# Optimization experiments

Hardware: AMD Instinct MI355X
Metric: run time of the kernel (lower is better)

The kernel has to match this reference:

```python
import jax, jax.numpy as jnp
import numpy as np

B, L, N = 8, 720, 321
D_MODEL, H, E_LAYERS, PRED = 512, 8, 2, 336
D_HEAD = D_MODEL // H
D_FF = 128
FACTOR = 5
U = min(int(FACTOR * np.ceil(np.log(L))), L)  # = 35: top-u queries and sample size
EPS = 1e-5


def _layer_norm(x, g, b):
    mu = x.mean(-1, keepdims=True)
    var = ((x - mu) ** 2).mean(-1, keepdims=True)
    return (x - mu) / jnp.sqrt(var + EPS) * g + b


def _prob_attention(q, k, v, samp_idx):
    # Informer ProbSparse attention (mask_flag=False). q,k,v: [B,H,L,Dh]
    Bq, Hq, Lq, Dh = q.shape
    k_samp = k[:, :, samp_idx, :]                                   # [B,H,L,S,Dh]
    qk_samp = jnp.einsum('bhld,bhlsd->bhls', q, k_samp)             # sampled scores
    M = qk_samp.max(-1) - qk_samp.sum(-1) / Lq                      # sparsity measure
    _, m_top = jax.lax.top_k(M, U)                                  # [B,H,U]
    q_red = jnp.take_along_axis(q, m_top[..., None], axis=2)        # [B,H,U,Dh]
    scores = jnp.einsum('bhud,bhld->bhul', q_red, k) * (1.0 / np.sqrt(Dh))
    attn = jax.nn.softmax(scores, axis=-1)
    upd = jnp.einsum('bhul,bhld->bhud', attn, v)                    # [B,H,U,Dh]
    ctx = jnp.broadcast_to(v.mean(axis=2, keepdims=True), q.shape)  # mean-V init
    b_idx = jnp.arange(Bq)[:, None, None]
    h_idx = jnp.arange(Hq)[None, :, None]
    return ctx.at[b_idx, h_idx, m_top].set(upd)


def _forward(x_enc, embed_w, embed_b, wq, bq, wk, bk, wv, bv, wo, bo,
             ln1_g, ln1_b, w1, b1, w2, b2, ln2_g, ln2_b,
             wout, bout, wg, bg, samp_idx):
    x = jnp.transpose(x_enc, (0, 2, 1))                             # [B,N,L]
    mean = x.mean(-1, keepdims=True)
    std = jnp.std(x, axis=-1, ddof=1, keepdims=True) + EPS
    xs = (x - mean) / std
    h = jnp.transpose(xs, (0, 2, 1)) @ embed_w + embed_b            # [B,L,Dm]
    y = jnp.zeros((B, L, PRED), dtype=h.dtype)

    def heads(t):
        return jnp.transpose(t.reshape(B, L, H, D_HEAD), (0, 2, 1, 3))

    for l in range(E_LAYERS):
        q = heads(h @ wq[l] + bq[l])
        k = heads(h @ wk[l] + bk[l])
        v = heads(h @ wv[l] + bv[l])
        ctx = _prob_attention(q, k, v, samp_idx)
        ctx = jnp.transpose(ctx, (0, 2, 1, 3)).reshape(B, L, D_MODEL)
        attn_out = ctx @ wo[l] + bo[l]
        hx = _layer_norm(h - attn_out, ln1_g[l], ln1_b[l])          # Minusformer subtraction
        ff = jax.nn.relu(hx @ w1[l] + b1[l]) @ w2[l] + b2[l]
        h = _layer_norm(hx - ff, ln2_g[l], ln2_b[l])
        y = y + (h @ wout[l] + bout[l]) * jax.nn.sigmoid(h @ wg[l] + bg[l])
    out = y[:, :N, :] * std + mean                                  # inverse scaling [B,N,PRED]
    return jnp.transpose(out, (0, 2, 1))                            # [B,PRED,N]


def setup_inputs() -> dict:
    key = jax.random.key(0)
    ks = jax.random.split(key, 12)
    s = 0.02

    def w(k, shape):
        return jax.random.normal(k, shape, dtype=jnp.float32) * s

    return {
        'x_enc': jax.random.normal(ks[0], (B, L, N), dtype=jnp.float32),
        'samp_idx': jax.random.randint(ks[1], (L, U), 0, L),
        'embed_w': w(ks[2], (N, D_MODEL)),
        'embed_b': jnp.zeros((D_MODEL,), jnp.float32),
        'wq': w(ks[3], (E_LAYERS, D_MODEL, D_MODEL)),
        'bq': jnp.zeros((E_LAYERS, D_MODEL), jnp.float32),
        'wk': w(ks[4], (E_LAYERS, D_MODEL, D_MODEL)),
        'bk': jnp.zeros((E_LAYERS, D_MODEL), jnp.float32),
        'wv': w(ks[5], (E_LAYERS, D_MODEL, D_MODEL)),
        'bv': jnp.zeros((E_LAYERS, D_MODEL), jnp.float32),
        'wo': w(ks[6], (E_LAYERS, D_MODEL, D_MODEL)),
        'bo': jnp.zeros((E_LAYERS, D_MODEL), jnp.float32),
        'ln1_g': jnp.ones((E_LAYERS, D_MODEL), jnp.float32),
        'ln1_b': jnp.zeros((E_LAYERS, D_MODEL), jnp.float32),
        'w1': w(ks[7], (E_LAYERS, D_MODEL, D_FF)),
        'b1': jnp.zeros((E_LAYERS, D_FF), jnp.float32),
        'w2': w(ks[8], (E_LAYERS, D_FF, D_MODEL)),
        'b2': jnp.zeros((E_LAYERS, D_MODEL), jnp.float32),
        'ln2_g': jnp.ones((E_LAYERS, D_MODEL), jnp.float32),
        'ln2_b': jnp.zeros((E_LAYERS, D_MODEL), jnp.float32),
        'wout': w(ks[9], (E_LAYERS, D_MODEL, PRED)),
        'bout': jnp.zeros((E_LAYERS, PRED), jnp.float32),
        'wg': w(ks[10], (E_LAYERS, D_MODEL, PRED)),
        'bg': jnp.zeros((E_LAYERS, PRED), jnp.float32),
    }


def reference(x_enc, samp_idx, embed_w, embed_b, wq, bq, wk, bk, wv, bv, wo, bo,
              ln1_g, ln1_b, w1, b1, w2, b2, ln2_g, ln2_b, wout, bout, wg, bg):
    return _forward(x_enc, embed_w, embed_b, wq, bq, wk, bk, wv, bv, wo, bo,
                    ln1_g, ln1_b, w1, b1, w2, b2, ln2_g, ln2_b,
                    wout, bout, wg, bg, samp_idx)
```

## Files before the change

kernel.cpp:

```cpp
#include <hip/hip_runtime.h>
#include <math.h>

#define BB_ 8
#define LL_ 720
#define NF 321
#define DM 512
#define HH_ 8
#define DH 64
#define DFF 128
#define PRED 336
#define UK 35
#define NLAY 2
#define EPSF 1e-5f
#define BL (BB_*LL_)
#define TJC 72
#define NCH (LL_/TJC)
#define LCH 48
#define NLC (LL_/LCH)

typedef unsigned short ushort;
typedef __attribute__((ext_vector_type(4))) float f32x4;
typedef __attribute__((ext_vector_type(8))) ushort ushort8;
typedef __attribute__((ext_vector_type(4))) ushort ushortx4;

#define KVSEG ((size_t)64*LL_*64)

__device__ __forceinline__ float b2f(ushort u){
  unsigned int x = ((unsigned int)u) << 16;
  return __builtin_bit_cast(float, x);
}
__device__ __forceinline__ ushort f2b(float f){
  unsigned int x = __builtin_bit_cast(unsigned int, f);
  unsigned int r = x + 0x7fff + ((x >> 16) & 1);
  return (ushort)(r >> 16);
}

__device__ __forceinline__ float wredsum(float v){
#pragma unroll
  for (int o=32;o>0;o>>=1) v += __shfl_xor(v,o,64);
  return v;
}
__device__ __forceinline__ float wredmax(float v){
#pragma unroll
  for (int o=32;o>0;o>>=1) v = fmaxf(v,__shfl_xor(v,o,64));
  return v;
}
__device__ __forceinline__ float bredsum(float v, float* red){
  int lane = threadIdx.x & 63, wid = threadIdx.x >> 6;
  v = wredsum(v);
  __syncthreads();
  if (lane==0) red[wid]=v;
  __syncthreads();
  return red[0]+red[1]+red[2]+red[3];
}

__global__ __launch_bounds__(256) void stats3_k(const float* __restrict__ x,
                                                float* __restrict__ pp){
  __shared__ float s1[4][64], s2[4][64];
  int blk = blockIdx.x;
  int lc = blk % NLC; int r = blk / NLC;
  int nt = r % 6; int b = r / 6;
  int nl = threadIdx.x & 63, lg = threadIdx.x >> 6;
  int n = nt*64 + nl;
  float sum=0.f, ss=0.f;
  if (n < NF){
    const float* xp = x + ((size_t)b*LL_ + lc*LCH)*NF + n;
    for (int l=lg; l<LCH; l+=4){ float v = xp[(size_t)l*NF]; sum += v; ss = fmaf(v,v,ss); }
  }
  s1[lg][nl]=sum; s2[lg][nl]=ss;
  __syncthreads();
  if (lg==0){
    float S = s1[0][nl]+s1[1][nl]+s1[2][nl]+s1[3][nl];
    float Q = s2[0][nl]+s2[1][nl]+s2[2][nl]+s2[3][nl];
    pp[(size_t)blk*128 + nl]      = S;
    pp[(size_t)blk*128 + 64 + nl] = Q;
  }
}

__global__ __launch_bounds__(64) void statsc_k(const float* __restrict__ pp,
                                               float* __restrict__ mean,
                                               float* __restrict__ stdv,
                                               float* __restrict__ rstd){
  int bn6 = blockIdx.x;
  int nl = threadIdx.x;
  int nt = bn6 % 6, b = bn6 / 6;
  int n = nt*64 + nl;
  if (n >= NF) return;
  float S=0.f, Q=0.f;
#pragma unroll
  for (int lc=0; lc<NLC; ++lc){
    size_t base = ((size_t)(b*6+nt)*NLC + lc)*128;
    S += pp[base + nl];
    Q += pp[base + 64 + nl];
  }
  float mu = S*(1.f/LL_);
  float var = fmaxf((Q - S*mu)*(1.f/(LL_-1)), 0.f);
  float sd = sqrtf(var) + EPSF;
  int bn = b*NF+n;
  mean[bn]=mu; stdv[bn]=sd; rstd[bn]=1.f/sd;
}

#define KPE 352
__global__ __launch_bounds__(256) void xnorm_k(const float* __restrict__ x,
                                               const float* __restrict__ mean,
                                               const float* __restrict__ rstd,
                                               ushort* __restrict__ xn){
  int idx = blockIdx.x*256 + threadIdx.x;
  if (idx >= BL*KPE) return;
  int c = idx % KPE; int bl = idx / KPE; int b = bl / LL_;
  float v = 0.f;
  if (c < NF) v = (x[(size_t)bl*NF + c] - mean[b*NF+c]) * rstd[b*NF+c];
  xn[idx] = f2b(v);
}

struct TDesc { const float* in; ushort* out; int N, K, Npad, Kpad, nbx, blk0, ilv; };
struct TPack { TDesc d[17]; int n; };
__global__ __launch_bounds__(256) void transpose_k(TPack p){
  __shared__ float tile[32][33];
  int blk = blockIdx.x;
  int di = 0;
  while (di+1 < p.n && p.d[di+1].blk0 <= blk) ++di;
  TDesc D = p.d[di];
  int rel = blk - D.blk0;
  int bx = rel % D.nbx, by = rel / D.nbx;
  int k0 = bx*32, n0 = by*32;
  int t = threadIdx.x; int tx = t & 31, ty = t >> 5;
#pragma unroll
  for (int i=0;i<4;++i){
    int k = k0+ty+8*i, n = n0+tx;
    float v = (k < D.K && n < D.N) ? D.in[(size_t)k*D.N + n] : 0.f;
    tile[ty+8*i][tx] = v;
  }
  __syncthreads();
#pragma unroll
  for (int i=0;i<4;++i){
    int n = n0+ty+8*i, k = k0+tx;
    if (n < D.Npad && k < D.Kpad){
      int outn = D.ilv ? (2*n + (D.ilv-1)) : n;
      D.out[(size_t)outn*D.Kpad + k] = f2b(tile[tx][ty+8*i]);
    }
  }
}

__global__ __launch_bounds__(256) void pack_bias_k(const float* __restrict__ bq,
                                                   const float* __restrict__ bk,
                                                   const float* __restrict__ bv,
                                                   const float* __restrict__ bo2,
                                                   const float* __restrict__ bg,
                                                   float* __restrict__ bqkv,
                                                   float* __restrict__ bog){
  int t = blockIdx.x*256 + threadIdx.x;
  if (t < 2*1536){
    int l = t/1536, c = t%1536;
    float v = c<512 ? bq[l*512+c] : (c<1024 ? bk[l*512+c-512] : bv[l*512+c-1024]);
    bqkv[t] = v;
  }
  if (t < 2*672){
    int l = t/672, c = t%672;
    int p = c>>1;
    bog[t] = (c&1) ? bg[l*336+p] : bo2[l*336+p];
  }
}

__global__ __launch_bounds__(256) void gemm_k(
    const ushort* __restrict__ A, const ushort* __restrict__ Bt,
    const float* __restrict__ bias, void* __restrict__ Cout,
    ushort* __restrict__ Cbf, ushort* __restrict__ kvp,
    int N, int K, int flags)
{
  __shared__ ushort As[128*32];
  __shared__ ushort Bs[128*32];
  const int t = threadIdx.x;
  const int bm = blockIdx.y << 7, bn = blockIdx.x << 7;
  const int lane = t & 63, wid = t >> 6;
  const int wm = (wid >> 1) << 6, wn = (wid & 1) << 6;
  const int fr = lane & 15, kg = lane >> 4;

  f32x4 acc[4][4];
#pragma unroll
  for (int i=0;i<4;++i)
#pragma unroll
    for (int j=0;j<4;++j) acc[i][j] = (f32x4){0.f,0.f,0.f,0.f};

  const int rA0 = t >> 2,        qA0 = t & 3;
  const int rA1 = (t+256) >> 2;
  const size_t aOff0 = (size_t)(bm + rA0)*K + qA0*8;
  const size_t aOff1 = (size_t)(bm + rA1)*K + qA0*8;
  const size_t bOff0 = (size_t)(bn + rA0)*K + qA0*8;
  const size_t bOff1 = (size_t)(bn + rA1)*K + qA0*8;
  const int lA0 = (rA0<<5) + ((qA0 ^ ((rA0>>1)&3))<<3);
  const int lA1 = (rA1<<5) + ((qA0 ^ ((rA1>>1)&3))<<3);

  for (int k0=0; k0<K; k0+=32){
    ushort8 va0 = *(const ushort8*)(A  + aOff0 + k0);
    ushort8 va1 = *(const ushort8*)(A  + aOff1 + k0);
    ushort8 vb0 = *(const ushort8*)(Bt + bOff0 + k0);
    ushort8 vb1 = *(const ushort8*)(Bt + bOff1 + k0);
    *(ushort8*)&As[lA0] = va0;
    *(ushort8*)&As[lA1] = va1;
    *(ushort8*)&Bs[lA0] = vb0;
    *(ushort8*)&Bs[lA1] = vb1;
    __syncthreads();
    ushort8 af[4], bfr[4];
#pragma unroll
    for (int i=0;i<4;++i){
      int ra = wm + (i<<4) + fr;
      af[i]  = *(const ushort8*)&As[(ra<<5) + ((kg ^ ((ra>>1)&3))<<3)];
      int rb = wn + (i<<4) + fr;
      bfr[i] = *(const ushort8*)&Bs[(rb<<5) + ((kg ^ ((rb>>1)&3))<<3)];
    }
#pragma unroll
    for (int i=0;i<4;++i)
#pragma unroll
      for (int j=0;j<4;++j)
        asm("v_mfma_f32_16x16x32_bf16 %0, %1, %2, %0"
            : "+v"(acc[i][j]) : "v"(af[i]), "v"(bfr[j]));
    __syncthreads();
  }

  const int colBase = bn + wn + fr;
  const int rowBase = bm + wm + (kg << 2);

  if (flags & 16){
#pragma unroll
    for (int j=0;j<4;++j){
      int col = colBase + (j<<4);
      if (col >= N) continue;
      float bv = bias[col];
#pragma unroll
      for (int i=0;i<4;++i){
        int row0 = rowBase + (i<<4);
#pragma unroll
        for (int r=0;r<4;++r){
          float v = acc[i][j][r] + bv;
          float o = __shfl_xor(v, 1, 64);
          if ((lane & 1) == 0){
            float val = v * (1.f/(1.f+__expf(-o)));
            size_t yi = (size_t)(row0+r)*PRED + (col>>1);
            float* yp = (float*)Cout;
            yp[yi] = (flags & 32) ? (yp[yi] + val) : val;
          }
        }
      }
    }
    return;
  }

#pragma unroll
  for (int j=0;j<4;++j){
    int col = colBase + (j<<4);
    if (col >= N) continue;
    float bv = bias[col];
#pragma unroll
    for (int i=0;i<4;++i){
      int row0 = rowBase + (i<<4);
#pragma unroll
      for (int r=0;r<4;++r){
        float v = acc[i][j][r] + bv;
        if (flags & 1) v = fmaxf(v, 0.f);
        int row = row0 + r;
        size_t idx = (size_t)row*N + col;
        if (flags & 2) ((ushort*)Cout)[idx] = f2b(v);
        else if (flags & 8){
          if (col < 512) ((float*)Cout)[idx] = v;
          else {
            int hh = (col >> 6) & 7;
            int dd = col & 63;
            int bb = row / LL_; int jr = row - bb*LL_;
            ushort bfv = f2b(v);
            if (col < 1024)
              kvp[((size_t)(bb*8+hh)*LL_ + jr)*64 + dd] = bfv;
            else
              kvp[KVSEG + ((size_t)(bb*8+hh)*LL_ + jr)*64 + dd] = bfv;
          }
        } else {
          ((float*)Cout)[idx] = v;
          if (flags & 4) Cbf[idx] = f2b(v);
        }
      }
    }
  }
}

__global__ __launch_bounds__(256) void msc_k(const float* __restrict__ qkv,
                                             const ushort* __restrict__ kR,
                                             const int* __restrict__ samp,
                                             float* __restrict__ Mb){
  __shared__ float sq[4][64];
  int wid = threadIdx.x >> 6, lane = threadIdx.x & 63;
  int gid = blockIdx.x*4 + wid;
  int l = gid % LL_; int bh = gid / LL_; int h = bh & 7; int b = bh >> 3;
  sq[wid][lane] = qkv[(size_t)(b*LL_ + l)*1536 + h*64 + lane];
  __syncthreads();
  float acc = 0.f;
  if (lane < UK){
    int j = samp[l*UK + lane];
    const ushort8* kr = (const ushort8*)(kR + ((size_t)bh*LL_ + j)*64);
    const float* sqw = sq[wid];
#pragma unroll
    for (int d8=0; d8<8; ++d8){
      ushort8 kk = kr[d8];
#pragma unroll
      for (int e=0;e<8;++e) acc = fmaf(sqw[d8*8+e], b2f(kk[e]), acc);
    }
  }
  float mx = (lane < UK) ? acc : -INFINITY;
  float sm = (lane < UK) ? acc : 0.f;
  mx = wredmax(mx);
  sm = wredsum(sm);
  if (lane == 0) Mb[gid] = mx - sm*(1.f/LL_);
}

__global__ __launch_bounds__(64) void topk2_k(const float* __restrict__ Mb,
                                              int* __restrict__ mtop){
  int bh = blockIdx.x; int lane = threadIdx.x;
  const float* mp = Mb + (size_t)bh*LL_;
  float v[12]; int vi[12];
#pragma unroll
  for (int i=0;i<12;++i){
    int j = lane + i*64;
    bool ok = j < LL_;
    v[i] = ok ? mp[j] : -INFINITY;
    vi[i] = ok ? j : (LL_ + i);
  }
  for (int it=0; it<UK; ++it){
    float best = v[0]; int bi = vi[0]; int bslot = 0;
#pragma unroll
    for (int i=1;i<12;++i){
      if (v[i] > best || (v[i]==best && vi[i] < bi)){ best=v[i]; bi=vi[i]; bslot=i; }
    }
    float gb = best; int gi = bi;
#pragma unroll
    for (int o=32;o>0;o>>=1){
      float ov = __shfl_xor(gb,o,64); int oi = __shfl_xor(gi,o,64);
      if (ov > gb || (ov==gb && oi < gi)){ gb=ov; gi=oi; }
    }
    if (lane==0) mtop[(size_t)bh*UK + it] = gi;
    if (bi == gi){
#pragma unroll
      for (int i=0;i<12;++i) if (i==bslot) v[i] = -INFINITY;
    }
  }
}

__global__ __launch_bounds__(256) void vmnc_k(const float* __restrict__ pvs,
                                              float* __restrict__ vmn){
  int idx = blockIdx.x*256 + threadIdx.x;
  if (idx >= 64*64) return;
  int bh = idx >> 6, d = idx & 63;
  float s = 0.f;
#pragma unroll
  for (int ch=0; ch<NCH; ++ch) s += pvs[((size_t)bh*NCH + ch)*64 + d];
  vmn[idx] = s*(1.f/LL_);
}

__global__ __launch_bounds__(256) void ctxfill_k(const float* __restrict__ vmn,
                                                 ushort* __restrict__ ctx){
  int idx = blockIdx.x*256 + threadIdx.x;
  int c4 = idx & 127; int bl = idx >> 7; int b = bl / LL_;
  int c = c4*4;
  const float* vm = vmn + (b*8 + (c>>6))*64 + (c&63);
  ushortx4 o = { f2b(vm[0]), f2b(vm[1]), f2b(vm[2]), f2b(vm[3]) };
  *(ushortx4*)&ctx[(size_t)bl*DM + c] = o;
}

__global__ __launch_bounds__(256) void attn4_k(const float* __restrict__ qkv,
                                               const ushort* __restrict__ kR,
                                               const ushort* __restrict__ vp,
                                               const int* __restrict__ mtop,
                                               float* __restrict__ pacc,
                                               float* __restrict__ pm,
                                               float* __restrict__ pl,
                                               float* __restrict__ pvs){
  __shared__ ushort skT[64][TJC];
  __shared__ ushort sv[TJC][64];
  __shared__ float  sq[UK][64];
  __shared__ float  sc[UK][TJC];
  __shared__ float  part[4][64];
  int blk = blockIdx.x;
  int ch = blk % NCH; int bh = blk / NCH;
  int b = bh >> 3, h = bh & 7; int t0 = ch*TJC;
  int t = threadIdx.x, lane = t & 63, wid = t >> 6;
  for (int idx=t; idx<TJC*8; idx+=256){
    int jj = idx>>3, c8 = idx&7;
    ushort8 kk = *(const ushort8*)(kR + ((size_t)bh*LL_ + t0+jj)*64 + c8*8);
#pragma unroll
    for (int e=0;e<8;++e) skT[c8*8+e][jj] = kk[e];
  }
  for (int idx=t; idx<TJC*8; idx+=256){
    int jj = idx>>3, c8 = idx&7;
    *(ushort8*)&sv[jj][c8*8] =
      *(const ushort8*)(vp + ((size_t)bh*LL_ + t0+jj)*64 + c8*8);
  }
  for (int idx=t; idx<UK*64; idx+=256){
    int u = idx>>6, d = idx&63;
    int row = mtop[bh*UK + u];
    sq[u][d] = qkv[(size_t)(b*LL_ + row)*1536 + h*64 + d];
  }
  __syncthreads();
  {
    int d = t & 63, q = t >> 6;
    float s = 0.f;
    for (int jj=q; jj<TJC; jj+=4) s += b2f(sv[jj][d]);
    part[q][d] = s;
  }
  for (int idx=t; idx<UK*(TJC/8); idx+=256){
    int u = idx/(TJC/8), jb = idx%(TJC/8);
    float dot[8] = {0.f,0.f,0.f,0.f,0.f,0.f,0.f,0.f};
    const float* qu = sq[u];
#pragma unroll
    for (int d=0; d<64; ++d){
      ushort8 kk = *(const ushort8*)&skT[d][jb*8];
      float qv = qu[d];
#pragma unroll
      for (int e=0;e<8;++e) dot[e] = fmaf(qv, b2f(kk[e]), dot[e]);
    }
#pragma unroll
    for (int e=0;e<8;++e) sc[u][jb*8+e] = dot[e]*0.125f;
  }
  __syncthreads();
  if (t < 64)
    pvs[((size_t)bh*NCH + ch)*64 + t] = part[0][t]+part[1][t]+part[2][t]+part[3][t];
  for (int u=wid; u<UK; u+=4){
    float v0 = sc[u][lane];
    float v1 = (lane < TJC-64) ? sc[u][64+lane] : -3.0e38f;
    float mx = wredmax(fmaxf(v0,v1));
    float e0 = __expf(v0-mx);
    float e1 = (lane < TJC-64) ? __expf(v1-mx) : 0.f;
    sc[u][lane] = e0;
    if (lane < TJC-64) sc[u][64+lane] = e1;
    float s = wredsum(e0+e1);
    if (lane==0){
      pm[((size_t)bh*NCH+ch)*UK + u] = mx;
      pl[((size_t)bh*NCH+ch)*UK + u] = s;
    }
  }
  __syncthreads();
  for (int idx=t; idx<UK*64; idx+=256){
    int u = idx>>6, d = idx&63;
    const float* scu = sc[u];
    float a = 0.f;
#pragma unroll 8
    for (int jj=0; jj<TJC; ++jj) a = fmaf(scu[jj], b2f(sv[jj][d]), a);
    pacc[(((size_t)bh*NCH+ch)*UK + u)*64 + d] = a;
  }
}

__global__ __launch_bounds__(256) void attn5_k(const float* __restrict__ pacc,
                                               const float* __restrict__ pm,
                                               const float* __restrict__ pl,
                                               const int* __restrict__ mtop,
                                               ushort* __restrict__ ctx){
  int bh = blockIdx.x; int b = bh >> 3, h = bh & 7;
  int t = threadIdx.x;
  for (int idx=t; idx<UK*64; idx+=256){
    int u = idx>>6, d = idx&63;
    float M = -3.0e38f;
#pragma unroll
    for (int ch=0; ch<NCH; ++ch)
      M = fmaxf(M, pm[((size_t)bh*NCH+ch)*UK + u]);
    float L = 0.f, A = 0.f;
#pragma unroll
    for (int ch=0; ch<NCH; ++ch){
      float w = __expf(pm[((size_t)bh*NCH+ch)*UK + u] - M);
      L += w * pl[((size_t)bh*NCH+ch)*UK + u];
      A += w * pacc[(((size_t)bh*NCH+ch)*UK + u)*64 + d];
    }
    int row = mtop[bh*UK + u];
    ctx[(size_t)(b*LL_ + row)*DM + h*64 + d] = f2b(A / L);
  }
}

__global__ __launch_bounds__(256) void subln_k(const float* __restrict__ a,
                                               const float* __restrict__ s,
                                               const float* __restrict__ g,
                                               const float* __restrict__ be,
                                               float* __restrict__ of32,
                                               ushort* __restrict__ obf){
  __shared__ float red[4];
  int row = blockIdx.x;
  size_t base = (size_t)row * DM;
  int t = threadIdx.x;
  float e0 = a[base+t]     - s[base+t];
  float e1 = a[base+t+256] - s[base+t+256];
  float sum = bredsum(e0+e1, red);
  float mu = sum * (1.f/DM);
  float d0 = e0-mu, d1 = e1-mu;
  __syncthreads();
  float var = bredsum(d0*d0+d1*d1, red);
  float rs = rsqrtf(var*(1.f/DM) + EPSF);
  float o0 = d0*rs*g[t]     + be[t];
  float o1 = d1*rs*g[t+256] + be[t+256];
  of32[base+t]     = o0;
  of32[base+t+256] = o1;
  obf[base+t]      = f2b(o0);
  obf[base+t+256]  = f2b(o1);
}

__global__ __launch_bounds__(256) void final2_k(const float* __restrict__ y,
                                                const float* __restrict__ stdv,
                                                const float* __restrict__ mean,
                                                float* __restrict__ out){
  __shared__ float tile[32][33];
  int n0 = blockIdx.x*32, p0 = blockIdx.y*32, b = blockIdx.z;
  int tx = threadIdx.x & 31, ty = threadIdx.x >> 5;
  for (int i=ty; i<32; i+=8){
    int n = n0+i, p = p0+tx;
    tile[i][tx] = (n<NF && p<PRED) ? y[((size_t)b*LL_+n)*PRED + p] : 0.f;
  }
  __syncthreads();
  for (int i=ty; i<32; i+=8){
    int p = p0+i, n = n0+tx;
    if (p<PRED && n<NF)
      out[((size_t)b*PRED + p)*NF + n] = tile[tx][i]*stdv[b*NF+n] + mean[b*NF+n];
  }
}

extern "C" void kernel_launch(void* const* d_in, const int* in_sizes, int n_in,
                              void* d_out, int out_size, void* d_ws, size_t ws_size,
                              hipStream_t stream){
  const float* x_enc = (const float*)d_in[0];
  const int*   samp  = (const int*)  d_in[1];
  const float* embw  = (const float*)d_in[2];
  const float* embb  = (const float*)d_in[3];
  const float* wq    = (const float*)d_in[4];
  const float* bq    = (const float*)d_in[5];
  const float* wk    = (const float*)d_in[6];
  const float* bk    = (const float*)d_in[7];
  const float* wv    = (const float*)d_in[8];
  const float* bv    = (const float*)d_in[9];
  const float* wo    = (const float*)d_in[10];
  const float* bo    = (const float*)d_in[11];
  const float* ln1g  = (const float*)d_in[12];
  const float* ln1b  = (const float*)d_in[13];
  const float* w1    = (const float*)d_in[14];
  const float* b1    = (const float*)d_in[15];
  const float* w2    = (const float*)d_in[16];
  const float* b2    = (const float*)d_in[17];
  const float* ln2g  = (const float*)d_in[18];
  const float* ln2b  = (const float*)d_in[19];
  const float* wout  = (const float*)d_in[20];
  const float* boutp = (const float*)d_in[21];
  const float* wg    = (const float*)d_in[22];
  const float* bg    = (const float*)d_in[23];
  float* out = (float*)d_out;

  char* wsb = (char*)d_ws;
  size_t off = 0;
  auto alloc = [&](size_t bytes)->void*{
    void* p = wsb + off; off += (bytes + 255) & ~(size_t)255; return p;
  };
  float* mean  = (float*)alloc((size_t)BB_*NF*4);
  float* stdv  = (float*)alloc((size_t)BB_*NF*4);
  float* rstd  = (float*)alloc((size_t)BB_*NF*4);
  float* pp    = (float*)alloc((size_t)BB_*6*NLC*128*4);
  float* bqkv  = (float*)alloc(2*1536*4);
  float* bog   = (float*)alloc(2*672*4);
  ushort* xn     = (ushort*)alloc((size_t)BL*KPE*2);
  ushort* we_t   = (ushort*)alloc((size_t)512*KPE*2);
  ushort* wqkv_t = (ushort*)alloc((size_t)2*1536*512*2);
  ushort* wo_t   = (ushort*)alloc((size_t)2*512*512*2);
  ushort* w1_t   = (ushort*)alloc((size_t)2*128*512*2);
  ushort* w2_t   = (ushort*)alloc((size_t)2*512*128*2);
  ushort* wog_t  = (ushort*)alloc((size_t)2*768*512*2);
  ushort* h_bf   = (ushort*)alloc((size_t)BL*DM*2);
  ushort* hx_bf  = (ushort*)alloc((size_t)BL*DM*2);
  ushort* ctx_bf = (ushort*)alloc((size_t)BL*DM*2);
  ushort* ff1_bf = (ushort*)alloc((size_t)BL*DFF*2);
  ushort* kvpack = (ushort*)alloc(2*KVSEG*2);
  float* h_f32   = (float*)alloc((size_t)BL*DM*4);
  float* hx_f32  = (float*)alloc((size_t)BL*DM*4);
  float* qkv = (float*)alloc((size_t)BL*1536*4);
  float* tmp = (float*)alloc((size_t)BL*DM*4);
  float* y   = (float*)alloc((size_t)BL*PRED*4);
  float* Mb  = (float*)alloc((size_t)BB_*HH_*LL_*4);
  int*  mtop = (int*)  alloc((size_t)BB_*HH_*UK*4);
  float* vmn = (float*)alloc((size_t)BB_*HH_*DH*4);
  float* pacc = (float*)alloc((size_t)64*NCH*UK*64*4);
  float* pm   = (float*)alloc((size_t)64*NCH*UK*4);
  float* pl   = (float*)alloc((size_t)64*NCH*UK*4);
  float* pvs  = (float*)alloc((size_t)64*NCH*64*4);
  if (off > ws_size) return;
  ushort* kRp   = kvpack;
  ushort* vpack = kvpack + KVSEG;

  stats3_k<<<BB_*6*NLC, 256, 0, stream>>>(x_enc, pp);
  statsc_k<<<BB_*6, 64, 0, stream>>>(pp, mean, stdv, rstd);
  xnorm_k<<<(BL*KPE+255)/256, 256, 0, stream>>>(x_enc, mean, rstd, xn);

  TPack tp; int blk = 0; int di = 0;
  auto addT = [&](const float* in, ushort* o, int N, int K, int Npad, int Kpad, int ilv){
    TDesc& d = tp.d[di++]; d.in=in; d.out=o; d.N=N; d.K=K; d.Npad=Npad; d.Kpad=Kpad; d.ilv=ilv;
    d.nbx = (Kpad+31)/32; d.blk0 = blk; blk += d.nbx * ((Npad+31)/32);
  };
  addT(embw, we_t, 512, NF, 512, KPE, 0);
  for (int l=0;l<NLAY;++l){
    addT(wq + (size_t)l*262144, wqkv_t + (size_t)l*786432,            512,512,512,512,0);
    addT(wk + (size_t)l*262144, wqkv_t + (size_t)l*786432 + 262144,   512,512,512,512,0);
    addT(wv + (size_t)l*262144, wqkv_t + (size_t)l*786432 + 524288,   512,512,512,512,0);
    addT(wo + (size_t)l*262144, wo_t   + (size_t)l*262144,            512,512,512,512,0);
    addT(w1 + (size_t)l*65536,  w1_t   + (size_t)l*65536,             128,512,128,512,0);
    addT(w2 + (size_t)l*65536,  w2_t   + (size_t)l*65536,             512,128,512,128,0);
    addT(wout + (size_t)l*172032, wog_t + (size_t)l*393216,           336,512,384,512,1);
    addT(wg   + (size_t)l*172032, wog_t + (size_t)l*393216,           336,512,384,512,2);
  }
  tp.n = di;
  transpose_k<<<blk, 256, 0, stream>>>(tp);
  pack_bias_k<<<12, 256, 0, stream>>>(bq, bk, bv, boutp, bg, bqkv, bog);

  gemm_k<<<dim3(4,45), 256, 0, stream>>>(xn, we_t, embb, h_f32, h_bf, nullptr,
                                         512, KPE, 4);

  for (int l=0;l<NLAY;++l){
    gemm_k<<<dim3(12,45), 256, 0, stream>>>(h_bf, wqkv_t + (size_t)l*786432,
                                            bqkv + l*1536, qkv, nullptr, kvpack,
                                            1536, 512, 8);
    msc_k<<<BB_*HH_*LL_/4, 256, 0, stream>>>(qkv, kRp, samp, Mb);
    topk2_k<<<BB_*HH_, 64, 0, stream>>>(Mb, mtop);
    attn4_k<<<64*NCH, 256, 0, stream>>>(qkv, kRp, vpack, mtop, pacc, pm, pl, pvs);
    vmnc_k<<<16, 256, 0, stream>>>(pvs, vmn);
    ctxfill_k<<<BL*DM/1024, 256, 0, stream>>>(vmn, ctx_bf);
    attn5_k<<<64, 256, 0, stream>>>(pacc, pm, pl, mtop, ctx_bf);
    gemm_k<<<dim3(4,45), 256, 0, stream>>>(ctx_bf, wo_t + (size_t)l*262144,
                                           bo + l*512, tmp, nullptr, nullptr,
                                           512, 512, 0);
    subln_k<<<BL, 256, 0, stream>>>(h_f32, tmp, ln1g + l*512, ln1b + l*512,
                                    hx_f32, hx_bf);
    gemm_k<<<dim3(1,45), 256, 0, stream>>>(hx_bf, w1_t + (size_t)l*65536,
                                           b1 + l*128, ff1_bf, nullptr, nullptr,
                                           128, 512, 3);
    gemm_k<<<dim3(4,45), 256, 0, stream>>>(ff1_bf, w2_t + (size_t)l*65536,
                                           b2 + l*512, tmp, nullptr, nullptr,
                                           512, 128, 0);
    subln_k<<<BL, 256, 0, stream>>>(hx_f32, tmp, ln2g + l*512, ln2b + l*512,
                                    h_f32, h_bf);
    gemm_k<<<dim3(6,45), 256, 0, stream>>>(h_bf, wog_t + (size_t)l*393216,
                                           bog + l*672, y, nullptr, nullptr,
                                           672, 512, 16 | (l ? 32 : 0));
  }
  final2_k<<<dim3((NF+31)/32,(PRED+31)/32,BB_), 256, 0, stream>>>(y, stdv, mean, out);
}
```

Baseline: 623.3 us.

## Drop fp32 residual copies, fuse context fill with merge, retile sampled scores

The residual stream is now kept only in bf16, so the fp32 h/hx buffers and their extra writes and reads go away. LayerNorm switches to a single-pass sum and sum-of-squares reduction. The mean-V fill and the top-u merge become one per-row kernel that uses a selection map written by top-k. The sparsity-measure kernel processes 8 queries per block with two keys per lane. These changes cut memory traffic and launches, but the bf16 residual and single-pass variance lose precision.

```diff
diff --git a/kernel.cpp b/kernel.cpp
--- a/kernel.cpp
+++ b/kernel.cpp
@@ -45,14 +45,6 @@
   for (int o=32;o>0;o>>=1) v = fmaxf(v,__shfl_xor(v,o,64));
   return v;
 }
-__device__ __forceinline__ float bredsum(float v, float* red){
-  int lane = threadIdx.x & 63, wid = threadIdx.x >> 6;
-  v = wredsum(v);
-  __syncthreads();
-  if (lane==0) red[wid]=v;
-  __syncthreads();
-  return red[0]+red[1]+red[2]+red[3];
-}
 
 __global__ __launch_bounds__(256) void stats3_k(const float* __restrict__ x,
                                                 float* __restrict__ pp){
@@ -165,7 +157,7 @@
 __global__ __launch_bounds__(256) void gemm_k(
     const ushort* __restrict__ A, const ushort* __restrict__ Bt,
     const float* __restrict__ bias, void* __restrict__ Cout,
-    ushort* __restrict__ Cbf, ushort* __restrict__ kvp,
+    ushort* __restrict__ kvp,
     int N, int K, int flags)
 {
   __shared__ ushort As[128*32];
@@ -275,46 +267,64 @@
           }
         } else {
           ((float*)Cout)[idx] = v;
-          if (flags & 4) Cbf[idx] = f2b(v);
         }
       }
     }
   }
 }
 
-__global__ __launch_bounds__(256) void msc_k(const float* __restrict__ qkv,
-                                             const ushort* __restrict__ kR,
-                                             const int* __restrict__ samp,
-                                             float* __restrict__ Mb){
-  __shared__ float sq[4][64];
-  int wid = threadIdx.x >> 6, lane = threadIdx.x & 63;
-  int gid = blockIdx.x*4 + wid;
-  int l = gid % LL_; int bh = gid / LL_; int h = bh & 7; int b = bh >> 3;
-  sq[wid][lane] = qkv[(size_t)(b*LL_ + l)*1536 + h*64 + lane];
-  __syncthreads();
-  float acc = 0.f;
-  if (lane < UK){
-    int j = samp[l*UK + lane];
-    const ushort8* kr = (const ushort8*)(kR + ((size_t)bh*LL_ + j)*64);
-    const float* sqw = sq[wid];
-#pragma unroll
-    for (int d8=0; d8<8; ++d8){
-      ushort8 kk = kr[d8];
-#pragma unroll
-      for (int e=0;e<8;++e) acc = fmaf(sqw[d8*8+e], b2f(kk[e]), acc);
-    }
-  }
-  float mx = (lane < UK) ? acc : -INFINITY;
-  float sm = (lane < UK) ? acc : 0.f;
-  mx = wredmax(mx);
-  sm = wredsum(sm);
-  if (lane == 0) Mb[gid] = mx - sm*(1.f/LL_);
+__global__ __launch_bounds__(256) void msc2_k(const float* __restrict__ qkv,
+                                              const ushort* __restrict__ kR,
+                                              const int* __restrict__ samp,
+                                              float* __restrict__ Mb){
+  __shared__ float sq[8][64];
+  __shared__ int sidx[8][UK];
+  int blk = blockIdx.x;
+  int l8 = blk % 90; int bh = blk / 90;
+  int b = bh >> 3, h = bh & 7; int l0 = l8*8;
+  int t = threadIdx.x;
+  for (int i=t; i<8*64; i+=256){
+    int u = i>>6, d = i&63;
+    sq[u][d] = qkv[(size_t)(b*LL_ + l0+u)*1536 + h*64 + d];
+  }
+  for (int i=t; i<8*UK; i+=256)
+    sidx[i/UK][i%UK] = samp[(l0 + i/UK)*UK + i%UK];
+  __syncthreads();
+  int g = t >> 5, gl = t & 31;
+  bool has1 = gl < (UK - 32);
+  int j0 = sidx[g][gl];
+  int j1 = has1 ? sidx[g][gl+32] : j0;
+  const ushort8* k0 = (const ushort8*)(kR + ((size_t)bh*LL_ + j0)*64);
+  const ushort8* k1 = (const ushort8*)(kR + ((size_t)bh*LL_ + j1)*64);
+  const float* qu = sq[g];
+  float a0 = 0.f, a1 = 0.f;
+#pragma unroll
+  for (int d8=0; d8<8; ++d8){
+    ushort8 x0 = k0[d8];
+    ushort8 x1 = k1[d8];
+#pragma unroll
+    for (int e=0;e<8;++e){
+      float q = qu[d8*8+e];
+      a0 = fmaf(q, b2f(x0[e]), a0);
+      a1 = fmaf(q, b2f(x1[e]), a1);
+    }
+  }
+  float mx = has1 ? fmaxf(a0, a1) : a0;
+  float sm = has1 ? (a0 + a1) : a0;
+#pragma unroll
+  for (int o=16;o>0;o>>=1){
+    mx = fmaxf(mx, __shfl_xor(mx, o, 32));
+    sm += __shfl_xor(sm, o, 32);
+  }
+  if (gl == 0) Mb[(size_t)bh*LL_ + l0 + g] = mx - sm*(1.f/LL_);
 }
 
 __global__ __launch_bounds__(64) void topk2_k(const float* __restrict__ Mb,
-                                              int* __restrict__ mtop){
+                                              int* __restrict__ mtop,
+                                              int* __restrict__ sel){
   int bh = blockIdx.x; int lane = threadIdx.x;
   const float* mp = Mb + (size_t)bh*LL_;
+  for (int j=lane; j<LL_; j+=64) sel[(size_t)bh*LL_ + j] = -1;
   float v[12]; int vi[12];
 #pragma unroll
   for (int i=0;i<12;++i){
@@ -335,7 +345,10 @@
       float ov = __shfl_xor(gb,o,64); int oi = __shfl_xor(gi,o,64);
       if (ov > gb || (ov==gb && oi < gi)){ gb=ov; gi=oi; }
     }
-    if (lane==0) mtop[(size_t)bh*UK + it] = gi;
+    if (lane==0){
+      mtop[(size_t)bh*UK + it] = gi;
+      sel[(size_t)bh*LL_ + gi] = it;
+    }
     if (bi == gi){
 #pragma unroll
       for (int i=0;i<12;++i) if (i==bslot) v[i] = -INFINITY;
@@ -352,16 +365,6 @@
 #pragma unroll
   for (int ch=0; ch<NCH; ++ch) s += pvs[((size_t)bh*NCH + ch)*64 + d];
   vmn[idx] = s*(1.f/LL_);
-}
-
-__global__ __launch_bounds__(256) void ctxfill_k(const float* __restrict__ vmn,
-                                                 ushort* __restrict__ ctx){
-  int idx = blockIdx.x*256 + threadIdx.x;
-  int c4 = idx & 127; int bl = idx >> 7; int b = bl / LL_;
-  int c = c4*4;
-  const float* vm = vmn + (b*8 + (c>>6))*64 + (c&63);
-  ushortx4 o = { f2b(vm[0]), f2b(vm[1]), f2b(vm[2]), f2b(vm[3]) };
-  *(ushortx4*)&ctx[(size_t)bl*DM + c] = o;
 }
 
 __global__ __launch_bounds__(256) void attn4_k(const float* __restrict__ qkv,
@@ -446,55 +449,71 @@
   }
 }
 
-__global__ __launch_bounds__(256) void attn5_k(const float* __restrict__ pacc,
-                                               const float* __restrict__ pm,
-                                               const float* __restrict__ pl,
-                                               const int* __restrict__ mtop,
-                                               ushort* __restrict__ ctx){
-  int bh = blockIdx.x; int b = bh >> 3, h = bh & 7;
+__global__ __launch_bounds__(256) void ctxw_k(const float* __restrict__ pacc,
+                                              const float* __restrict__ pm,
+                                              const float* __restrict__ pl,
+                                              const float* __restrict__ vmn,
+                                              const int* __restrict__ sel,
+                                              ushort* __restrict__ ctx){
+  int bl = blockIdx.x;
+  int b = bl / LL_; int l = bl - b*LL_;
   int t = threadIdx.x;
-  for (int idx=t; idx<UK*64; idx+=256){
-    int u = idx>>6, d = idx&63;
-    float M = -3.0e38f;
-#pragma unroll
-    for (int ch=0; ch<NCH; ++ch)
-      M = fmaxf(M, pm[((size_t)bh*NCH+ch)*UK + u]);
-    float L = 0.f, A = 0.f;
-#pragma unroll
-    for (int ch=0; ch<NCH; ++ch){
-      float w = __expf(pm[((size_t)bh*NCH+ch)*UK + u] - M);
-      L += w * pl[((size_t)bh*NCH+ch)*UK + u];
-      A += w * pacc[(((size_t)bh*NCH+ch)*UK + u)*64 + d];
-    }
-    int row = mtop[bh*UK + u];
-    ctx[(size_t)(b*LL_ + row)*DM + h*64 + d] = f2b(A / L);
-  }
-}
-
-__global__ __launch_bounds__(256) void subln_k(const float* __restrict__ a,
+  for (int c=t; c<DM; c+=256){
+    int h = c >> 6, d = c & 63;
+    int bh = b*8 + h;
+    int u = sel[(size_t)bh*LL_ + l];
+    float val;
+    if (u < 0){
+      val = vmn[bh*64 + d];
+    } else {
+      float pmv[NCH];
+      float M = -3.0e38f;
+#pragma unroll
+      for (int ch=0; ch<NCH; ++ch){
+        pmv[ch] = pm[((size_t)bh*NCH+ch)*UK + u];
+        M = fmaxf(M, pmv[ch]);
+      }
+      float L = 0.f, A = 0.f;
+#pragma unroll
+      for (int ch=0; ch<NCH; ++ch){
+        float w = __expf(pmv[ch] - M);
+        L += w * pl[((size_t)bh*NCH+ch)*UK + u];
+        A += w * pacc[(((size_t)bh*NCH+ch)*UK + u)*64 + d];
+      }
+      val = A / L;
+    }
+    ctx[(size_t)bl*DM + c] = f2b(val);
+  }
+}
+
+__global__ __launch_bounds__(256) void subln_k(const ushort* __restrict__ a,
                                                const float* __restrict__ s,
                                                const float* __restrict__ g,
                                                const float* __restrict__ be,
-                                               float* __restrict__ of32,
                                                ushort* __restrict__ obf){
-  __shared__ float red[4];
+  __shared__ float red[8];
   int row = blockIdx.x;
   size_t base = (size_t)row * DM;
   int t = threadIdx.x;
-  float e0 = a[base+t]     - s[base+t];
-  float e1 = a[base+t+256] - s[base+t+256];
-  float sum = bredsum(e0+e1, red);
-  float mu = sum * (1.f/DM);
-  float d0 = e0-mu, d1 = e1-mu;
-  __syncthreads();
-  float var = bredsum(d0*d0+d1*d1, red);
-  float rs = rsqrtf(var*(1.f/DM) + EPSF);
-  float o0 = d0*rs*g[t]     + be[t];
-  float o1 = d1*rs*g[t+256] + be[t+256];
-  of32[base+t]     = o0;
-  of32[base+t+256] = o1;
-  obf[base+t]      = f2b(o0);
-  obf[base+t+256]  = f2b(o1);
+  int lane = t & 63, wid = t >> 6;
+  float e0 = b2f(a[base+t])     - s[base+t];
+  float e1 = b2f(a[base+t+256]) - s[base+t+256];
+  float s1 = e0+e1;
+  float s2 = e0*e0 + e1*e1;
+#pragma unroll
+  for (int o=32;o>0;o>>=1){
+    s1 += __shfl_xor(s1,o,64);
+    s2 += __shfl_xor(s2,o,64);
+  }
+  if (lane==0){ red[wid]=s1; red[4+wid]=s2; }
+  __syncthreads();
+  float S = red[0]+red[1]+red[2]+red[3];
+  float Q = red[4]+red[5]+red[6]+red[7];
+  float mu = S*(1.f/DM);
+  float var = fmaxf(Q*(1.f/DM) - mu*mu, 0.f);
+  float rs = rsqrtf(var + EPSF);
+  obf[base+t]     = f2b((e0-mu)*rs*g[t]     + be[t]);
+  obf[base+t+256] = f2b((e1-mu)*rs*g[t+256] + be[t+256]);
 }
 
 __global__ __launch_bounds__(256) void final2_k(const float* __restrict__ y,
@@ -568,13 +587,12 @@
   ushort* ctx_bf = (ushort*)alloc((size_t)BL*DM*2);
   ushort* ff1_bf = (ushort*)alloc((size_t)BL*DFF*2);
   ushort* kvpack = (ushort*)alloc(2*KVSEG*2);
-  float* h_f32   = (float*)alloc((size_t)BL*DM*4);
-  float* hx_f32  = (float*)alloc((size_t)BL*DM*4);
   float* qkv = (float*)alloc((size_t)BL*1536*4);
   float* tmp = (float*)alloc((size_t)BL*DM*4);
   float* y   = (float*)alloc((size_t)BL*PRED*4);
   float* Mb  = (float*)alloc((size_t)BB_*HH_*LL_*4);
   int*  mtop = (int*)  alloc((size_t)BB_*HH_*UK*4);
+  int*  sel  = (int*)  alloc((size_t)BB_*HH_*LL_*4);
   float* vmn = (float*)alloc((size_t)BB_*HH_*DH*4);
   float* pacc = (float*)alloc((size_t)64*NCH*UK*64*4);
   float* pm   = (float*)alloc((size_t)64*NCH*UK*4);
@@ -608,34 +626,31 @@
   transpose_k<<<blk, 256, 0, stream>>>(tp);
   pack_bias_k<<<12, 256, 0, stream>>>(bq, bk, bv, boutp, bg, bqkv, bog);
 
-  gemm_k<<<dim3(4,45), 256, 0, stream>>>(xn, we_t, embb, h_f32, h_bf, nullptr,
-                                         512, KPE, 4);
+  gemm_k<<<dim3(4,45), 256, 0, stream>>>(xn, we_t, embb, h_bf, nullptr,
+                                         512, KPE, 2);
 
   for (int l=0;l<NLAY;++l){
     gemm_k<<<dim3(12,45), 256, 0, stream>>>(h_bf, wqkv_t + (size_t)l*786432,
-                                            bqkv + l*1536, qkv, nullptr, kvpack,
+                                            bqkv + l*1536, qkv, kvpack,
                                             1536, 512, 8);
-    msc_k<<<BB_*HH_*LL_/4, 256, 0, stream>>>(qkv, kRp, samp, Mb);
-    topk2_k<<<BB_*HH_, 64, 0, stream>>>(Mb, mtop);
+    msc2_k<<<64*90, 256, 0, stream>>>(qkv, kRp, samp, Mb);
+    topk2_k<<<BB_*HH_, 64, 0, stream>>>(Mb, mtop, sel);
     attn4_k<<<64*NCH, 256, 0, stream>>>(qkv, kRp, vpack, mtop, pacc, pm, pl, pvs);
     vmnc_k<<<16, 256, 0, stream>>>(pvs, vmn);
-    ctxfill_k<<<BL*DM/1024, 256, 0, stream>>>(vmn, ctx_bf);
-    attn5_k<<<64, 256, 0, stream>>>(pacc, pm, pl, mtop, ctx_bf);
+    ctxw_k<<<BL, 256, 0, stream>>>(pacc, pm, pl, vmn, sel, ctx_bf);
     gemm_k<<<dim3(4,45), 256, 0, stream>>>(ctx_bf, wo_t + (size_t)l*262144,
-                                           bo + l*512, tmp, nullptr, nullptr,
+                                           bo + l*512, tmp, nullptr,
                                            512, 512, 0);
-    subln_k<<<BL, 256, 0, stream>>>(h_f32, tmp, ln1g + l*512, ln1b + l*512,
-                                    hx_f32, hx_bf);
+    subln_k<<<BL, 256, 0, stream>>>(h_bf, tmp, ln1g + l*512, ln1b + l*512, hx_bf);
     gemm_k<<<dim3(1,45), 256, 0, stream>>>(hx_bf, w1_t + (size_t)l*65536,
-                                           b1 + l*128, ff1_bf, nullptr, nullptr,
+                                           b1 + l*128, ff1_bf, nullptr,
                                            128, 512, 3);
     gemm_k<<<dim3(4,45), 256, 0, stream>>>(ff1_bf, w2_t + (size_t)l*65536,
-                                           b2 + l*512, tmp, nullptr, nullptr,
+                                           b2 + l*512, tmp, nullptr,
                                            512, 128, 0);
-    subln_k<<<BL, 256, 0, stream>>>(hx_f32, tmp, ln2g + l*512, ln2b + l*512,
-                                    h_f32, h_bf);
+    subln_k<<<BL, 256, 0, stream>>>(hx_bf, tmp, ln2g + l*512, ln2b + l*512, h_bf);
     gemm_k<<<dim3(6,45), 256, 0, stream>>>(h_bf, wog_t + (size_t)l*393216,
-                                           bog + l*672, y, nullptr, nullptr,
+                                           bog + l*672, y, nullptr,
                                            672, 512, 16 | (l ? 32 : 0));
   }
   final2_k<<<dim3((NF+31)/32,(PRED+31)/32,BB_), 256, 0, stream>>>(y, stdv, mean, out);
```

Result: slower. 642.5 us (+3.1%).
